# Kernel tuning notes

Hardware: AMD Instinct MI355X
Metric: run time of the kernel (lower is better)

## Reference

```python
import jax, jax.numpy as jnp
import numpy as np

B, CIN, COUT, N, K, S, NLEV = 2, 32, 32, 131072, 27, 3, 6

def setup_inputs() -> dict:
    key = jax.random.key(0)
    k1, k2, k3, k4, k5 = jax.random.split(key, 5)
    input_features = jax.random.normal(k1, (B, CIN, N), dtype=jnp.float32)
    # learned params (kaiming-uniform-ish scale)
    fan_in = CIN * 3 * 3 * 3
    bound = 1.0 / np.sqrt(fan_in)
    weight = jax.random.uniform(k2, (CIN, S, COUT, 3, 3, 3), dtype=jnp.float32,
                                minval=-bound, maxval=bound)
    bias = jax.random.uniform(k3, (COUT,), dtype=jnp.float32, minval=-bound, maxval=bound)
    # APR surrogate: precomputed 27-point neighborhood per particle + octree level
    neighbor_idx = jax.random.randint(k4, (N, K), 0, N)
    levels = jax.random.randint(k5, (N,), 0, NLEV)
    level_deltas = jnp.zeros((B,), dtype=jnp.int64 if jax.config.jax_enable_x64 else jnp.int32)
    return {"input_features": input_features, "weight": weight, "bias": bias,
            "neighbor_idx": neighbor_idx, "levels": levels, "level_deltas": level_deltas}

def reference(input_features, weight, bias, neighbor_idx, levels, level_deltas):
    # input_features: [B, Cin, N]; weight: [Cin, S, Cout, 3,3,3]
    Cin, nS, Cout = weight.shape[0], weight.shape[1], weight.shape[2]
    w = weight.reshape(Cin, nS, Cout, K)  # flatten 3x3x3 stencil -> 27
    # stencil selection per (batch, particle): level shifted by per-batch delta,
    # clamped to available stencils (kernel restriction modeled as clamp)
    sidx = jnp.clip(levels[None, :] + level_deltas[:, None], 0, nS - 1)  # [B, N]
    # irregular gather over the adaptive particle neighborhood
    x_nbr = input_features[:, :, neighbor_idx]  # [B, Cin, N, 27]
    out = jnp.zeros((input_features.shape[0], Cout, input_features.shape[2]),
                    dtype=input_features.dtype)
    for s in range(nS):  # small fixed stencil count
        y = jnp.einsum('bcnk,cok->bon', x_nbr, w[:, s])  # [B, Cout, N]
        out = out + jnp.where((sidx == s)[:, None, :], y, 0.0)
    return out + bias[None, :, None]
```

## Files before the change

### kernel.cpp

```cpp
#include <hip/hip_runtime.h>
#include <hip/hip_bf16.h>

#define N_PTS 131072
#define CIN   32
#define COUT  32
#define KNB   27
#define NS    3

typedef __bf16 bf16x8 __attribute__((ext_vector_type(8)));
typedef float  f32x4  __attribute__((ext_vector_type(4)));

__device__ __attribute__((aligned(256))) __bf16 g_xT[(size_t)N_PTS * 64];
__device__ __attribute__((aligned(256))) __bf16 g_wp[NS * COUT * 864];

__global__ void pack_x(const float* __restrict__ x) {
  int n = blockIdx.x * 256 + threadIdx.x;
  uint u[32];
#pragma unroll
  for (int b = 0; b < 2; ++b)
#pragma unroll
    for (int c = 0; c < 32; c += 2) {
      float f0 = x[(size_t)(b * 32 + c) * N_PTS + n];
      float f1 = x[(size_t)(b * 32 + c + 1) * N_PTS + n];
      union { __bf16 h[2]; uint w; } cv;
      cv.h[0] = (__bf16)f0; cv.h[1] = (__bf16)f1;
      u[b * 16 + c / 2] = cv.w;
    }
  uint4* dst = reinterpret_cast<uint4*>(&g_xT[(size_t)n * 64]);
#pragma unroll
  for (int i = 0; i < 8; ++i)
    dst[i] = make_uint4(u[4 * i], u[4 * i + 1], u[4 * i + 2], u[4 * i + 3]);
}

__global__ void pack_w(const float* __restrict__ w) {
  int e = blockIdx.x * 256 + threadIdx.x;
  int c  = e & 31;
  int kc = (e >> 5) % 27;
  int so = e / 864;
  int o  = so & 31;
  int s  = so >> 5;
  g_wp[e] = (__bf16)w[((size_t)(c * NS + s) * COUT + o) * KNB + kc];
}

__global__ __launch_bounds__(256, 4) void aprconv(
    const int* __restrict__ nbr, const int* __restrict__ levels,
    const int* __restrict__ deltas, const float* __restrict__ bias,
    float* __restrict__ out) {

  __shared__ int   s_idx[KNB * 64];
  __shared__ int   s_lv[64];
  __shared__ float s_bias[COUT];
  __shared__ __attribute__((aligned(16))) __bf16 s_w[2][96 * 40];

  const int tid = threadIdx.x;
  const int n0  = blockIdx.x * 64;
  const int wv  = tid >> 6;
  const int l15 = tid & 15;
  const int lg  = (tid & 63) >> 4;

  for (int j = tid; j < 64 * KNB; j += 256) {
    int p = j / KNB, kc = j - p * KNB;
    s_idx[kc * 64 + p] = nbr[(size_t)(n0 + p) * KNB + kc];
  }
  if (tid < 64) s_lv[tid]  = levels[n0 + tid];
  if (tid < COUT) s_bias[tid] = bias[tid];

  {
    const char* wp = (const char*)g_wp;
    char* dst = (char*)&s_w[0][0];
    { int r = tid >> 2, seg = tid & 3;
      *(uint4*)(dst + r * 80 + seg * 16) = *(const uint4*)(wp + r * 1728 + seg * 16); }
    if (tid < 128) { int q = tid + 256; int r = q >> 2, seg = q & 3;
      *(uint4*)(dst + r * 80 + seg * 16) = *(const uint4*)(wp + r * 1728 + seg * 16); }
  }
  __syncthreads();

  const int d0 = deltas[0], d1 = deltas[1];

  f32x4 acc[2][3][2];
#pragma unroll
  for (int b = 0; b < 2; ++b)
#pragma unroll
    for (int s = 0; s < 3; ++s)
#pragma unroll
      for (int ot = 0; ot < 2; ++ot)
        acc[b][s][ot] = (f32x4){0.f, 0.f, 0.f, 0.f};

  const char* xbase = (const char*)g_xT;
  bf16x8 xf0, xf1;
  {
    int idv = s_idx[wv * 16 + l15];
    xf0 = *(const bf16x8*)(xbase + (size_t)idv * 128 + lg * 16);
    xf1 = *(const bf16x8*)(xbase + (size_t)idv * 128 + 64 + lg * 16);
  }

  for (int kc = 0; kc < KNB; ++kc) {
    const int cur = kc & 1;
    bf16x8 wf[3][2];
    const char* wb = (const char*)&s_w[cur][0];
#pragma unroll
    for (int s = 0; s < 3; ++s)
#pragma unroll
      for (int ot = 0; ot < 2; ++ot)
        wf[s][ot] = *(const bf16x8*)(wb + (s * 32 + ot * 16 + l15) * 80 + lg * 16);

    bf16x8 xn0, xn1; uint4 ws0, ws1;
    const bool last = (kc == KNB - 1);
    if (!last) {
      int idn = s_idx[(kc + 1) * 64 + wv * 16 + l15];
      xn0 = *(const bf16x8*)(xbase + (size_t)idn * 128 + lg * 16);
      xn1 = *(const bf16x8*)(xbase + (size_t)idn * 128 + 64 + lg * 16);
      const char* wp = (const char*)g_wp;
      { int r = tid >> 2, seg = tid & 3;
        ws0 = *(const uint4*)(wp + r * 1728 + (kc + 1) * 64 + seg * 16); }
      if (tid < 128) { int q = tid + 256; int r = q >> 2, seg = q & 3;
        ws1 = *(const uint4*)(wp + r * 1728 + (kc + 1) * 64 + seg * 16); }
    }

#pragma unroll
    for (int s = 0; s < 3; ++s)
#pragma unroll
      for (int ot = 0; ot < 2; ++ot) {
        acc[0][s][ot] = __builtin_amdgcn_mfma_f32_16x16x32_bf16(wf[s][ot], xf0, acc[0][s][ot], 0, 0, 0);
        acc[1][s][ot] = __builtin_amdgcn_mfma_f32_16x16x32_bf16(wf[s][ot], xf1, acc[1][s][ot], 0, 0, 0);
      }

    if (!last) {
      char* dst = (char*)&s_w[cur ^ 1][0];
      { int r = tid >> 2, seg = tid & 3;
        *(uint4*)(dst + r * 80 + seg * 16) = ws0; }
      if (tid < 128) { int q = tid + 256; int r = q >> 2, seg = q & 3;
        *(uint4*)(dst + r * 80 + seg * 16) = ws1; }
      xf0 = xn0; xf1 = xn1;
    }
    __syncthreads();
  }

  const int p  = wv * 16 + l15;
  const int lv = s_lv[p];
  int e0 = lv + d0; e0 = e0 < 0 ? 0 : (e0 > 2 ? 2 : e0);
  int e1 = lv + d1; e1 = e1 < 0 ? 0 : (e1 > 2 ? 2 : e1);
  const int n = n0 + p;
#pragma unroll
  for (int b = 0; b < 2; ++b) {
    const int sb = b ? e1 : e0;
#pragma unroll
    for (int ot = 0; ot < 2; ++ot) {
      f32x4 a0 = acc[b][0][ot], a1 = acc[b][1][ot], a2 = acc[b][2][ot];
      f32x4 v;
#pragma unroll
      for (int r = 0; r < 4; ++r)
        v[r] = (sb == 0) ? a0[r] : ((sb == 1) ? a1[r] : a2[r]);
#pragma unroll
      for (int r = 0; r < 4; ++r) {
        int o = ot * 16 + lg * 4 + r;
        out[(size_t)(b * COUT + o) * N_PTS + n] = v[r] + s_bias[o];
      }
    }
  }
}

extern "C" void kernel_launch(void* const* d_in, const int* in_sizes, int n_in,
                              void* d_out, int out_size, void* d_ws, size_t ws_size,
                              hipStream_t stream) {
  const float* x    = (const float*)d_in[0];
  const float* w    = (const float*)d_in[1];
  const float* bias = (const float*)d_in[2];
  const int* nbr    = (const int*)d_in[3];
  const int* lv     = (const int*)d_in[4];
  const int* dlt    = (const int*)d_in[5];
  float* out        = (float*)d_out;

  hipLaunchKernelGGL(pack_x, dim3(N_PTS / 256), dim3(256), 0, stream, x);
  hipLaunchKernelGGL(pack_w, dim3((NS * COUT * 864) / 256), dim3(256), 0, stream, w);
  hipLaunchKernelGGL(aprconv, dim3(N_PTS / 64), dim3(256), 0, stream, nbr, lv, dlt, bias, out);
}
```

Measured before the change: 99.36 us.

## Load weights directly from global per lane and deepen gather prefetch

Weights are repacked as [kc][s][o][c] so each lane reads its MFMA weight fragments straight from global/L2, removing the LDS double buffer and the per-iteration __syncthreads. The neighbor gather is now prefetched two stencil taps ahead, and weights one tap ahead, with the loop unrolled by 3. This removes barrier stalls and LDS traffic, at the cost of more global loads (the weights are small and cached) and higher register pressure.

```diff
diff --git a/kernel.cpp b/kernel.cpp
--- a/kernel.cpp
+++ b/kernel.cpp
@@ -11,7 +11,7 @@
 typedef float  f32x4  __attribute__((ext_vector_type(4)));
 
 __device__ __attribute__((aligned(256))) __bf16 g_xT[(size_t)N_PTS * 64];
-__device__ __attribute__((aligned(256))) __bf16 g_wp[NS * COUT * 864];
+__device__ __attribute__((aligned(256))) __bf16 g_wp[KNB * NS * COUT * CIN];
 
 __global__ void pack_x(const float* __restrict__ x) {
   int n = blockIdx.x * 256 + threadIdx.x;
@@ -35,10 +35,9 @@
 __global__ void pack_w(const float* __restrict__ w) {
   int e = blockIdx.x * 256 + threadIdx.x;
   int c  = e & 31;
-  int kc = (e >> 5) % 27;
-  int so = e / 864;
-  int o  = so & 31;
-  int s  = so >> 5;
+  int o  = (e >> 5) & 31;
+  int s  = (e >> 10) % 3;
+  int kc = e / 3072;
   g_wp[e] = (__bf16)w[((size_t)(c * NS + s) * COUT + o) * KNB + kc];
 }
 
@@ -50,32 +49,26 @@
   __shared__ int   s_idx[KNB * 64];
   __shared__ int   s_lv[64];
   __shared__ float s_bias[COUT];
-  __shared__ __attribute__((aligned(16))) __bf16 s_w[2][96 * 40];
 
   const int tid = threadIdx.x;
   const int n0  = blockIdx.x * 64;
   const int wv  = tid >> 6;
   const int l15 = tid & 15;
   const int lg  = (tid & 63) >> 4;
+  const int slot = wv * 16 + l15;
 
   for (int j = tid; j < 64 * KNB; j += 256) {
     int p = j / KNB, kc = j - p * KNB;
     s_idx[kc * 64 + p] = nbr[(size_t)(n0 + p) * KNB + kc];
   }
-  if (tid < 64) s_lv[tid]  = levels[n0 + tid];
+  if (tid < 64)   s_lv[tid]   = levels[n0 + tid];
   if (tid < COUT) s_bias[tid] = bias[tid];
-
-  {
-    const char* wp = (const char*)g_wp;
-    char* dst = (char*)&s_w[0][0];
-    { int r = tid >> 2, seg = tid & 3;
-      *(uint4*)(dst + r * 80 + seg * 16) = *(const uint4*)(wp + r * 1728 + seg * 16); }
-    if (tid < 128) { int q = tid + 256; int r = q >> 2, seg = q & 3;
-      *(uint4*)(dst + r * 80 + seg * 16) = *(const uint4*)(wp + r * 1728 + seg * 16); }
-  }
   __syncthreads();
 
   const int d0 = deltas[0], d1 = deltas[1];
+
+  const char* xbase = (const char*)g_xT;
+  const char* wlane = (const char*)g_wp + (l15 << 6) + (lg << 4);
 
   f32x4 acc[2][3][2];
 #pragma unroll
@@ -86,57 +79,56 @@
       for (int ot = 0; ot < 2; ++ot)
         acc[b][s][ot] = (f32x4){0.f, 0.f, 0.f, 0.f};
 
-  const char* xbase = (const char*)g_xT;
-  bf16x8 xf0, xf1;
+  bf16x8 xa0, xa1, xc0, xc1, wa[3][2];
   {
-    int idv = s_idx[wv * 16 + l15];
-    xf0 = *(const bf16x8*)(xbase + (size_t)idv * 128 + lg * 16);
-    xf1 = *(const bf16x8*)(xbase + (size_t)idv * 128 + 64 + lg * 16);
-  }
-
-  for (int kc = 0; kc < KNB; ++kc) {
-    const int cur = kc & 1;
-    bf16x8 wf[3][2];
-    const char* wb = (const char*)&s_w[cur][0];
+    int i0 = s_idx[slot];
+    const char* p0 = xbase + ((uint)i0 << 7) + (lg << 4);
+    xa0 = *(const bf16x8*)p0;  xa1 = *(const bf16x8*)(p0 + 64);
+    int i1 = s_idx[64 + slot];
+    const char* p1 = xbase + ((uint)i1 << 7) + (lg << 4);
+    xc0 = *(const bf16x8*)p1;  xc1 = *(const bf16x8*)(p1 + 64);
 #pragma unroll
     for (int s = 0; s < 3; ++s)
 #pragma unroll
       for (int ot = 0; ot < 2; ++ot)
-        wf[s][ot] = *(const bf16x8*)(wb + (s * 32 + ot * 16 + l15) * 80 + lg * 16);
+        wa[s][ot] = *(const bf16x8*)(wlane + (s * 32 + ot * 16) * 64);
+  }
 
-    bf16x8 xn0, xn1; uint4 ws0, ws1;
-    const bool last = (kc == KNB - 1);
-    if (!last) {
-      int idn = s_idx[(kc + 1) * 64 + wv * 16 + l15];
-      xn0 = *(const bf16x8*)(xbase + (size_t)idn * 128 + lg * 16);
-      xn1 = *(const bf16x8*)(xbase + (size_t)idn * 128 + 64 + lg * 16);
-      const char* wp = (const char*)g_wp;
-      { int r = tid >> 2, seg = tid & 3;
-        ws0 = *(const uint4*)(wp + r * 1728 + (kc + 1) * 64 + seg * 16); }
-      if (tid < 128) { int q = tid + 256; int r = q >> 2, seg = q & 3;
-        ws1 = *(const uint4*)(wp + r * 1728 + (kc + 1) * 64 + seg * 16); }
+#pragma unroll 3
+  for (int kc = 0; kc < KNB; ++kc) {
+    const int kn1 = (kc + 1 < KNB) ? kc + 1 : KNB - 1;
+    const int kn2 = (kc + 2 < KNB) ? kc + 2 : KNB - 1;
+
+    bf16x8 wn[3][2], xn0, xn1;
+    const char* wp = wlane + kn1 * 6144;
+#pragma unroll
+    for (int s = 0; s < 3; ++s)
+#pragma unroll
+      for (int ot = 0; ot < 2; ++ot)
+        wn[s][ot] = *(const bf16x8*)(wp + (s * 32 + ot * 16) * 64);
+    {
+      int i2 = s_idx[kn2 * 64 + slot];
+      const char* p2 = xbase + ((uint)i2 << 7) + (lg << 4);
+      xn0 = *(const bf16x8*)p2;  xn1 = *(const bf16x8*)(p2 + 64);
     }
 
 #pragma unroll
     for (int s = 0; s < 3; ++s)
 #pragma unroll
       for (int ot = 0; ot < 2; ++ot) {
-        acc[0][s][ot] = __builtin_amdgcn_mfma_f32_16x16x32_bf16(wf[s][ot], xf0, acc[0][s][ot], 0, 0, 0);
-        acc[1][s][ot] = __builtin_amdgcn_mfma_f32_16x16x32_bf16(wf[s][ot], xf1, acc[1][s][ot], 0, 0, 0);
+        acc[0][s][ot] = __builtin_amdgcn_mfma_f32_16x16x32_bf16(wa[s][ot], xa0, acc[0][s][ot], 0, 0, 0);
+        acc[1][s][ot] = __builtin_amdgcn_mfma_f32_16x16x32_bf16(wa[s][ot], xa1, acc[1][s][ot], 0, 0, 0);
       }
 
-    if (!last) {
-      char* dst = (char*)&s_w[cur ^ 1][0];
-      { int r = tid >> 2, seg = tid & 3;
-        *(uint4*)(dst + r * 80 + seg * 16) = ws0; }
-      if (tid < 128) { int q = tid + 256; int r = q >> 2, seg = q & 3;
-        *(uint4*)(dst + r * 80 + seg * 16) = ws1; }
-      xf0 = xn0; xf1 = xn1;
-    }
-    __syncthreads();
+#pragma unroll
+    for (int s = 0; s < 3; ++s)
+#pragma unroll
+      for (int ot = 0; ot < 2; ++ot)
+        wa[s][ot] = wn[s][ot];
+    xa0 = xc0; xa1 = xc1; xc0 = xn0; xc1 = xn1;
   }
 
-  const int p  = wv * 16 + l15;
+  const int p  = slot;
   const int lv = s_lv[p];
   int e0 = lv + d0; e0 = e0 < 0 ? 0 : (e0 > 2 ? 2 : e0);
   int e1 = lv + d1; e1 = e1 < 0 ? 0 : (e1 > 2 ? 2 : e1);
@@ -172,6 +164,6 @@
   float* out        = (float*)d_out;
 
   hipLaunchKernelGGL(pack_x, dim3(N_PTS / 256), dim3(256), 0, stream, x);
-  hipLaunchKernelGGL(pack_w, dim3((NS * COUT * 864) / 256), dim3(256), 0, stream, w);
+  hipLaunchKernelGGL(pack_w, dim3((KNB * NS * COUT * CIN) / 256), dim3(256), 0, stream, w);
   hipLaunchKernelGGL(aprconv, dim3(N_PTS / 64), dim3(256), 0, stream, nbr, lv, dlt, bias, out);
 }
```

After: 162.9 us. 1.64x slower.
